# Kernel optimization log

Hardware: AMD Instinct MI355X
Metric: run time of the kernel (lower is better)

## Reference

```python
import jax, jax.numpy as jnp
import numpy as np

T, H = 4096, 2048

def _glorot(key, shape):
    return jax.random.uniform(key, shape, minval=-1.0, maxval=1.0) * jnp.sqrt(2.0 / sum(shape))

def setup_inputs() -> dict:
    key = jax.random.key(0)
    kx, ka, kb = jax.random.split(key, 3)
    x = jax.random.normal(kx, (T, H), dtype=jnp.float32)
    a_mat = _glorot(ka, (H,)).astype(jnp.float32)          # |a| < 1 -> stable recurrence
    b_mat = _glorot(kb, (H, H)).astype(jnp.float32)
    return {"x": x, "a_mat": a_mat, "b_mat": b_mat}

def reference(x, a_mat, b_mat):
    # s_t = b_mat.T @ x_t for all t, done as one GEMM: (T,H) @ (H,H)
    s = x @ b_mat  # (T, H)
    def step(h, s_t):
        h = jnp.tanh(a_mat * h + s_t)
        return h, h
    h0 = jnp.zeros_like(a_mat)
    _, h_seq = jax.lax.scan(step, h0, s)
    return h_seq  # (T, H)
```

## Files before the change

kernel.cpp:

```cpp
#include <hip/hip_runtime.h>
#include <stdint.h>
#include <stddef.h>

#define Tdim 4096
#define Hdim 2048

typedef short short8 __attribute__((ext_vector_type(8)));
typedef float floatx4 __attribute__((ext_vector_type(4)));

__device__ __forceinline__ unsigned short f2bf(float f) {
  uint32_t u = __float_as_uint(f);
  u += 0x7fffu + ((u >> 16) & 1u);
  return (unsigned short)(u >> 16);
}

__device__ __forceinline__ void load_lds16(const void* g, void* l) {
  __builtin_amdgcn_global_load_lds(
      (__attribute__((address_space(1))) unsigned int*)(uintptr_t)g,
      (__attribute__((address_space(3))) unsigned int*)l,
      16, 0, 0);
}

__device__ __forceinline__ float tanh_fast(float z) {
  float e = __expf(z + z);
  return 1.0f - __fdividef(2.0f, e + 1.0f);
}

__device__ __forceinline__ short8 lds_read8(const unsigned short* p) {
  return *(const short8*)__builtin_assume_aligned(p, 16);
}

__global__ __launch_bounds__(256) void cvt_kernel(const float* __restrict__ x,
                                                  const float* __restrict__ b,
                                                  unsigned short* __restrict__ xbf,
                                                  unsigned short* __restrict__ bt) {
  __shared__ unsigned short tile[64 * 65];
  const int t = threadIdx.x;
  if (blockIdx.x < 4096) {
    size_t i = ((size_t)blockIdx.x * 256 + t) * 8;
    float4 f0 = *(const float4*)(x + i);
    float4 f1 = *(const float4*)(x + i + 4);
    union { unsigned short u[8]; uint4 v; } o;
    o.u[0] = f2bf(f0.x); o.u[1] = f2bf(f0.y); o.u[2] = f2bf(f0.z); o.u[3] = f2bf(f0.w);
    o.u[4] = f2bf(f1.x); o.u[5] = f2bf(f1.y); o.u[6] = f2bf(f1.z); o.u[7] = f2bf(f1.w);
    *(uint4*)(xbf + i) = o.v;
    return;
  }
  const int tb = blockIdx.x - 4096;
  const int bj = tb & 31;
  const int bi = tb >> 5;
  {
    const int r0 = t >> 4, c4 = (t & 15) * 4;
#pragma unroll
    for (int p = 0; p < 4; ++p) {
      int r = r0 + p * 16;
      float4 v = *(const float4*)(b + (size_t)(bi * 64 + r) * Hdim + bj * 64 + c4);
      tile[r * 65 + c4 + 0] = f2bf(v.x);
      tile[r * 65 + c4 + 1] = f2bf(v.y);
      tile[r * 65 + c4 + 2] = f2bf(v.z);
      tile[r * 65 + c4 + 3] = f2bf(v.w);
    }
  }
  __syncthreads();
  {
    const int n = t >> 2, kq = (t & 3) * 16;
    union { unsigned short u[16]; uint4 v[2]; } o;
#pragma unroll
    for (int q = 0; q < 16; ++q) o.u[q] = tile[(kq + q) * 65 + n];
    uint4* dst = (uint4*)(bt + (size_t)(bj * 64 + n) * Hdim + bi * 64 + kq);
    dst[0] = o.v[0];
    dst[1] = o.v[1];
  }
}

__global__ __launch_bounds__(256) void gemm_scan_kernel(const unsigned short* __restrict__ A,
                                                        const unsigned short* __restrict__ Bt,
                                                        const float* __restrict__ a_mat,
                                                        float* __restrict__ out) {
  __shared__ alignas(16) union SM {
    struct {
      unsigned short sA[2][128 * 64];
      unsigned short sB[2][128 * 64];
      unsigned short sAw[2][8 * 64];
    } st;
    float s_tile[136 * 129];
  } sm;

  const int tid = threadIdx.x;
  const int bm = blockIdx.x, bn = blockIdx.y;
  const int wave = tid >> 6, lane = tid & 63;
  const int wm = (wave >> 1) * 64, wn = (wave & 1) * 64;
  const int l15 = lane & 15, quad = lane >> 4;
  const int l7 = l15 & 7;

  const int swz = ((tid & 7) ^ ((tid >> 3) & 7)) * 8;
  const unsigned short* aSrc = A + ((size_t)(bm * 128 + (tid >> 3)) * Hdim + swz);
  const unsigned short* bSrc = Bt + ((size_t)(bn * 128 + (tid >> 3)) * Hdim + swz);
  const int tw0 = (bm > 0) ? bm * 128 - 8 : 0;
  const int wswz = ((lane & 7) ^ ((lane >> 3) & 7)) * 8;
  const unsigned short* wSrc = A + ((size_t)(tw0 + (lane >> 3)) * Hdim + wswz);

  floatx4 acc[4][4] = {};
  floatx4 accw[4] = {};

  auto stage = [&](int buf, int k0) {
    unsigned short* aDst = &sm.st.sA[buf][tid * 8];
    unsigned short* bDst = &sm.st.sB[buf][tid * 8];
#pragma unroll
    for (int c = 0; c < 4; ++c)
      load_lds16(aSrc + (size_t)c * 32 * Hdim + k0, aDst + c * 2048);
#pragma unroll
    for (int c = 0; c < 4; ++c)
      load_lds16(bSrc + (size_t)c * 32 * Hdim + k0, bDst + c * 2048);
    if (wave == 3) load_lds16(wSrc + k0, &sm.st.sAw[buf][lane * 8]);
  };

  auto compute = [&](int buf) {
#pragma unroll
    for (int kk = 0; kk < 64; kk += 32) {
      const int coff = (((kk >> 3) + quad) ^ l7) * 8;
      short8 av[4], bv[4];
#pragma unroll
      for (int i = 0; i < 4; ++i)
        av[i] = lds_read8(&sm.st.sA[buf][(wm + i * 16 + l15) * 64 + coff]);
#pragma unroll
      for (int j = 0; j < 4; ++j)
        bv[j] = lds_read8(&sm.st.sB[buf][(wn + j * 16 + l15) * 64 + coff]);
#pragma unroll
      for (int i = 0; i < 4; ++i)
#pragma unroll
        for (int j = 0; j < 4; ++j)
          acc[i][j] = __builtin_amdgcn_mfma_f32_16x16x32_bf16(av[i], bv[j], acc[i][j], 0, 0, 0);
      if (wave < 2) {
        short8 aw = lds_read8(&sm.st.sAw[buf][l7 * 64 + coff]);
#pragma unroll
        for (int j = 0; j < 4; ++j)
          accw[j] = __builtin_amdgcn_mfma_f32_16x16x32_bf16(aw, bv[j], accw[j], 0, 0, 0);
      }
    }
  };

  stage(0, 0);
  __syncthreads();
  for (int it = 0; it < 32; it += 2) {
    stage(1, (it + 1) * 64);
    compute(0);
    __syncthreads();
    if (it + 2 < 32) stage(0, (it + 2) * 64);
    compute(1);
    __syncthreads();
  }

  if (wave < 2 && quad < 2) {
#pragma unroll
    for (int j = 0; j < 4; ++j)
#pragma unroll
      for (int r = 0; r < 4; ++r)
        sm.s_tile[(quad * 4 + r) * 129 + wn + j * 16 + l15] = accw[j][r];
  }
#pragma unroll
  for (int i = 0; i < 4; ++i)
#pragma unroll
    for (int j = 0; j < 4; ++j)
#pragma unroll
      for (int r = 0; r < 4; ++r)
        sm.s_tile[(8 + wm + i * 16 + quad * 4 + r) * 129 + wn + j * 16 + l15] = acc[i][j][r];
  __syncthreads();

  const int col = tid & 127;
  const int half = tid >> 7;
  const float aj = a_mat[bn * 128 + col];
  float h = 0.0f;
  const int row0 = 8 + half * 64;
  if (!(bm == 0 && half == 0)) {
#pragma unroll
    for (int r = row0 - 8; r < row0; ++r)
      h = tanh_fast(fmaf(aj, h, sm.s_tile[r * 129 + col]));
  }
  const size_t gbase = (size_t)(bm * 128 + half * 64) * Hdim + bn * 128 + col;
#pragma unroll 4
  for (int r2 = 0; r2 < 64; ++r2) {
    h = tanh_fast(fmaf(aj, h, sm.s_tile[(row0 + r2) * 129 + col]));
    out[gbase + (size_t)r2 * Hdim] = h;
  }
}

extern "C" void kernel_launch(void* const* d_in, const int* in_sizes, int n_in,
                              void* d_out, int out_size, void* d_ws, size_t ws_size,
                              hipStream_t stream) {
  const float* x = (const float*)d_in[0];
  const float* a = (const float*)d_in[1];
  const float* b = (const float*)d_in[2];
  float* out = (float*)d_out;

  unsigned short* ws = (unsigned short*)d_ws;
  unsigned short* xbf = ws;
  unsigned short* btb = xbf + (size_t)Tdim * Hdim;

  hipLaunchKernelGGL(cvt_kernel, dim3(4096 + (Hdim / 64) * (Hdim / 64)), dim3(256), 0, stream,
                     x, b, xbf, btb);
  hipLaunchKernelGGL(gemm_scan_kernel, dim3(Tdim / 128, Hdim / 128), dim3(256), 0, stream,
                     xbf, btb, a, out);
}
```

Before: 139.7 us.

## Enlarge GEMM tile to 256x128 with triple-buffered LDS pipeline and remapped grid

The fused GEMM+scan kernel moves to 512 threads with a 256x128 output tile and a three-stage LDS buffer. Global-to-LDS prefetch is split into two halves interleaved with the two k-substeps, synchronized by raw s_barrier and explicit vmcnt/lgkmcnt waits, and MFMA sections run at raised priority. Block indices are remapped to a 1D grid with a swizzle meant to improve L2 reuse. The aim is to overlap loads with MFMA work and to re-read B less often. The cost is much larger LDS use and register pressure that may limit occupancy, plus fragile hand-written wait counts.

```diff
diff --git a/kernel.cpp b/kernel.cpp
--- a/kernel.cpp
+++ b/kernel.cpp
@@ -73,83 +73,134 @@
   }
 }
 
-__global__ __launch_bounds__(256) void gemm_scan_kernel(const unsigned short* __restrict__ A,
-                                                        const unsigned short* __restrict__ Bt,
-                                                        const float* __restrict__ a_mat,
-                                                        float* __restrict__ out) {
+#define BARM() asm volatile("s_barrier" ::: "memory")
+#define WAITV(N) asm volatile("s_waitcnt vmcnt(" #N ")" ::: "memory")
+#define WAITL0() asm volatile("s_waitcnt lgkmcnt(0)" ::: "memory")
+
+__global__ __launch_bounds__(512, 2) void gemm_scan_kernel(const unsigned short* __restrict__ A,
+                                                           const unsigned short* __restrict__ Bt,
+                                                           const float* __restrict__ a_mat,
+                                                           float* __restrict__ out) {
   __shared__ alignas(16) union SM {
     struct {
-      unsigned short sA[2][128 * 64];
-      unsigned short sB[2][128 * 64];
-      unsigned short sAw[2][8 * 64];
+      unsigned short sA[3][256 * 64];
+      unsigned short sB[3][128 * 64];
+      unsigned short sAw[3][8 * 64];
     } st;
-    float s_tile[136 * 129];
+    float s_tile[264 * 129];
   } sm;
 
   const int tid = threadIdx.x;
-  const int bm = blockIdx.x, bn = blockIdx.y;
+  const int b0 = blockIdx.x;
+  const int nid = (b0 & 7) * 32 + (b0 >> 3);
+  const int bm = nid >> 4;
+  const int bn = nid & 15;
   const int wave = tid >> 6, lane = tid & 63;
   const int wm = (wave >> 1) * 64, wn = (wave & 1) * 64;
   const int l15 = lane & 15, quad = lane >> 4;
   const int l7 = l15 & 7;
 
   const int swz = ((tid & 7) ^ ((tid >> 3) & 7)) * 8;
-  const unsigned short* aSrc = A + ((size_t)(bm * 128 + (tid >> 3)) * Hdim + swz);
+  const unsigned short* aSrc = A + ((size_t)(bm * 256 + (tid >> 3)) * Hdim + swz);
   const unsigned short* bSrc = Bt + ((size_t)(bn * 128 + (tid >> 3)) * Hdim + swz);
-  const int tw0 = (bm > 0) ? bm * 128 - 8 : 0;
+  const int tw0 = (bm > 0) ? bm * 256 - 8 : 0;
   const int wswz = ((lane & 7) ^ ((lane >> 3) & 7)) * 8;
   const unsigned short* wSrc = A + ((size_t)(tw0 + (lane >> 3)) * Hdim + wswz);
 
   floatx4 acc[4][4] = {};
   floatx4 accw[4] = {};
 
-  auto stage = [&](int buf, int k0) {
-    unsigned short* aDst = &sm.st.sA[buf][tid * 8];
-    unsigned short* bDst = &sm.st.sB[buf][tid * 8];
-#pragma unroll
-    for (int c = 0; c < 4; ++c)
-      load_lds16(aSrc + (size_t)c * 32 * Hdim + k0, aDst + c * 2048);
-#pragma unroll
-    for (int c = 0; c < 4; ++c)
-      load_lds16(bSrc + (size_t)c * 32 * Hdim + k0, bDst + c * 2048);
-    if (wave == 3) load_lds16(wSrc + k0, &sm.st.sAw[buf][lane * 8]);
+  const int c0 = (quad ^ l7) * 8;
+  const int c1 = c0 ^ 32;
+  int rA[4], rB[4];
+#pragma unroll
+  for (int i = 0; i < 4; ++i) rA[i] = (wm + i * 16 + l15) * 64;
+#pragma unroll
+  for (int j = 0; j < 4; ++j) rB[j] = (wn + j * 16 + l15) * 64;
+
+  auto stage_p0 = [&](int nb, int k0) {
+    unsigned short* aDst = &sm.st.sA[nb][tid * 8];
+    load_lds16(aSrc + k0, aDst);
+    load_lds16(aSrc + (size_t)64 * Hdim + k0, aDst + 4096);
+    load_lds16(bSrc + k0, &sm.st.sB[nb][tid * 8]);
   };
-
-  auto compute = [&](int buf) {
-#pragma unroll
-    for (int kk = 0; kk < 64; kk += 32) {
-      const int coff = (((kk >> 3) + quad) ^ l7) * 8;
-      short8 av[4], bv[4];
-#pragma unroll
-      for (int i = 0; i < 4; ++i)
-        av[i] = lds_read8(&sm.st.sA[buf][(wm + i * 16 + l15) * 64 + coff]);
-#pragma unroll
-      for (int j = 0; j < 4; ++j)
-        bv[j] = lds_read8(&sm.st.sB[buf][(wn + j * 16 + l15) * 64 + coff]);
-#pragma unroll
-      for (int i = 0; i < 4; ++i)
-#pragma unroll
-        for (int j = 0; j < 4; ++j)
-          acc[i][j] = __builtin_amdgcn_mfma_f32_16x16x32_bf16(av[i], bv[j], acc[i][j], 0, 0, 0);
-      if (wave < 2) {
-        short8 aw = lds_read8(&sm.st.sAw[buf][l7 * 64 + coff]);
-#pragma unroll
-        for (int j = 0; j < 4; ++j)
-          accw[j] = __builtin_amdgcn_mfma_f32_16x16x32_bf16(aw, bv[j], accw[j], 0, 0, 0);
-      }
-    }
+  auto stage_p1 = [&](int nb, int k0) {
+    unsigned short* aDst = &sm.st.sA[nb][tid * 8];
+    load_lds16(aSrc + (size_t)128 * Hdim + k0, aDst + 8192);
+    load_lds16(aSrc + (size_t)192 * Hdim + k0, aDst + 12288);
+    load_lds16(bSrc + (size_t)64 * Hdim + k0, &sm.st.sB[nb][tid * 8 + 4096]);
+    if (wave == 7) load_lds16(wSrc + k0, &sm.st.sAw[nb][lane * 8]);
   };
 
-  stage(0, 0);
+  stage_p0(0, 0);  stage_p1(0, 0);
+  stage_p0(1, 64); stage_p1(1, 64);
+  if (wave == 7) { WAITV(7); } else { WAITV(6); }
+  BARM();
+
+  int buf = 0;
+  for (int t = 0; t < 32; ++t) {
+    const int nb = (buf >= 1) ? buf - 1 : 2;
+    const bool pf = (t < 30);
+    const int k2 = (t + 2) * 64;
+    const unsigned short* sAb = sm.st.sA[buf];
+    const unsigned short* sBb = sm.st.sB[buf];
+    const unsigned short* sWb = sm.st.sAw[buf];
+
+    short8 av[4], bv[4], aw = {};
+
+#pragma unroll
+    for (int i = 0; i < 4; ++i) av[i] = lds_read8(sAb + rA[i] + c0);
+#pragma unroll
+    for (int j = 0; j < 4; ++j) bv[j] = lds_read8(sBb + rB[j] + c0);
+    if (wave < 2) aw = lds_read8(sWb + l7 * 64 + c0);
+    if (pf) stage_p0(nb, k2);
+    BARM();
+    WAITL0();
+    __builtin_amdgcn_sched_barrier(0);
+    __builtin_amdgcn_s_setprio(1);
+#pragma unroll
+    for (int i = 0; i < 4; ++i)
+#pragma unroll
+      for (int j = 0; j < 4; ++j)
+        acc[i][j] = __builtin_amdgcn_mfma_f32_16x16x32_bf16(av[i], bv[j], acc[i][j], 0, 0, 0);
+    if (wave < 2) {
+#pragma unroll
+      for (int j = 0; j < 4; ++j)
+        accw[j] = __builtin_amdgcn_mfma_f32_16x16x32_bf16(aw, bv[j], accw[j], 0, 0, 0);
+    }
+    __builtin_amdgcn_s_setprio(0);
+    BARM();
+
+#pragma unroll
+    for (int i = 0; i < 4; ++i) av[i] = lds_read8(sAb + rA[i] + c1);
+#pragma unroll
+    for (int j = 0; j < 4; ++j) bv[j] = lds_read8(sBb + rB[j] + c1);
+    if (wave < 2) aw = lds_read8(sWb + l7 * 64 + c1);
+    if (pf) stage_p1(nb, k2);
+    BARM();
+    WAITL0();
+    __builtin_amdgcn_sched_barrier(0);
+    __builtin_amdgcn_s_setprio(1);
+#pragma unroll
+    for (int i = 0; i < 4; ++i)
+#pragma unroll
+      for (int j = 0; j < 4; ++j)
+        acc[i][j] = __builtin_amdgcn_mfma_f32_16x16x32_bf16(av[i], bv[j], acc[i][j], 0, 0, 0);
+    if (wave < 2) {
+#pragma unroll
+      for (int j = 0; j < 4; ++j)
+        accw[j] = __builtin_amdgcn_mfma_f32_16x16x32_bf16(aw, bv[j], accw[j], 0, 0, 0);
+    }
+    __builtin_amdgcn_s_setprio(0);
+    if (t < 30) {
+      if (wave == 7) { WAITV(7); } else { WAITV(6); }
+    } else if (t == 30) {
+      WAITV(0);
+    }
+    BARM();
+    buf = (buf == 2) ? 0 : buf + 1;
+  }
   __syncthreads();
-  for (int it = 0; it < 32; it += 2) {
-    stage(1, (it + 1) * 64);
-    compute(0);
-    __syncthreads();
-    if (it + 2 < 32) stage(0, (it + 2) * 64);
-    compute(1);
-    __syncthreads();
-  }
 
   if (wave < 2 && quad < 2) {
 #pragma unroll
@@ -168,16 +219,16 @@
   __syncthreads();
 
   const int col = tid & 127;
-  const int half = tid >> 7;
+  const int chunk = tid >> 7;
   const float aj = a_mat[bn * 128 + col];
   float h = 0.0f;
-  const int row0 = 8 + half * 64;
-  if (!(bm == 0 && half == 0)) {
+  const int row0 = 8 + chunk * 64;
+  if (!(bm == 0 && chunk == 0)) {
 #pragma unroll
     for (int r = row0 - 8; r < row0; ++r)
       h = tanh_fast(fmaf(aj, h, sm.s_tile[r * 129 + col]));
   }
-  const size_t gbase = (size_t)(bm * 128 + half * 64) * Hdim + bn * 128 + col;
+  const size_t gbase = (size_t)(bm * 256 + chunk * 64) * Hdim + bn * 128 + col;
 #pragma unroll 4
   for (int r2 = 0; r2 < 64; ++r2) {
     h = tanh_fast(fmaf(aj, h, sm.s_tile[(row0 + r2) * 129 + col]));
@@ -199,6 +250,6 @@
 
   hipLaunchKernelGGL(cvt_kernel, dim3(4096 + (Hdim / 64) * (Hdim / 64)), dim3(256), 0, stream,
                      x, b, xbf, btb);
-  hipLaunchKernelGGL(gemm_scan_kernel, dim3(Tdim / 128, Hdim / 128), dim3(256), 0, stream,
+  hipLaunchKernelGGL(gemm_scan_kernel, dim3((Tdim / 256) * (Hdim / 128)), dim3(512), 0, stream,
                      xbf, btb, a, out);
 }
```

New measurement: 142.2 us. Within noise of the previous version (+1.8%).

## Load B fragments directly from global into registers, drop B LDS staging

Applied to the files above, without the earlier changes.

The B operand no longer goes through LDS. Each wave reads its own B fragments straight from global memory into registers, double-buffered across k-steps, and launch bounds now request 2 blocks per CU. This halves staging LDS traffic and lets more blocks fit per CU. In exchange B is no longer shared between the two waves that use the same columns, so global and L2 traffic goes up, and the 16 extra short8 registers per thread may cause spills under the tighter occupancy bound.

```diff
diff --git a/kernel.cpp b/kernel.cpp
--- a/kernel.cpp
+++ b/kernel.cpp
@@ -27,6 +27,9 @@
 }
 
 __device__ __forceinline__ short8 lds_read8(const unsigned short* p) {
+  return *(const short8*)__builtin_assume_aligned(p, 16);
+}
+__device__ __forceinline__ short8 glb_read8(const unsigned short* p) {
   return *(const short8*)__builtin_assume_aligned(p, 16);
 }
 
@@ -73,14 +76,13 @@
   }
 }
 
-__global__ __launch_bounds__(256) void gemm_scan_kernel(const unsigned short* __restrict__ A,
-                                                        const unsigned short* __restrict__ Bt,
-                                                        const float* __restrict__ a_mat,
-                                                        float* __restrict__ out) {
+__global__ __launch_bounds__(256, 2) void gemm_scan_kernel(const unsigned short* __restrict__ A,
+                                                           const unsigned short* __restrict__ Bt,
+                                                           const float* __restrict__ a_mat,
+                                                           float* __restrict__ out) {
   __shared__ alignas(16) union SM {
     struct {
       unsigned short sA[2][128 * 64];
-      unsigned short sB[2][128 * 64];
       unsigned short sAw[2][8 * 64];
     } st;
     float s_tile[136 * 129];
@@ -95,59 +97,70 @@
 
   const int swz = ((tid & 7) ^ ((tid >> 3) & 7)) * 8;
   const unsigned short* aSrc = A + ((size_t)(bm * 128 + (tid >> 3)) * Hdim + swz);
-  const unsigned short* bSrc = Bt + ((size_t)(bn * 128 + (tid >> 3)) * Hdim + swz);
   const int tw0 = (bm > 0) ? bm * 128 - 8 : 0;
   const int wswz = ((lane & 7) ^ ((lane >> 3) & 7)) * 8;
   const unsigned short* wSrc = A + ((size_t)(tw0 + (lane >> 3)) * Hdim + wswz);
 
+  const unsigned short* bBase = Bt + ((size_t)(bn * 128 + wn + l15) * Hdim + quad * 8);
+
   floatx4 acc[4][4] = {};
   floatx4 accw[4] = {};
 
   auto stage = [&](int buf, int k0) {
     unsigned short* aDst = &sm.st.sA[buf][tid * 8];
-    unsigned short* bDst = &sm.st.sB[buf][tid * 8];
 #pragma unroll
     for (int c = 0; c < 4; ++c)
       load_lds16(aSrc + (size_t)c * 32 * Hdim + k0, aDst + c * 2048);
-#pragma unroll
-    for (int c = 0; c < 4; ++c)
-      load_lds16(bSrc + (size_t)c * 32 * Hdim + k0, bDst + c * 2048);
     if (wave == 3) load_lds16(wSrc + k0, &sm.st.sAw[buf][lane * 8]);
   };
 
-  auto compute = [&](int buf) {
+  auto loadB = [&](short8 (&dst)[8], int k0) {
+#pragma unroll
+    for (int j = 0; j < 4; ++j) {
+      const unsigned short* p = bBase + (size_t)(j * 16) * Hdim + k0;
+      dst[j * 2 + 0] = glb_read8(p);
+      dst[j * 2 + 1] = glb_read8(p + 32);
+    }
+  };
+
+  auto compute = [&](int buf, const short8 (&bv)[8]) {
 #pragma unroll
     for (int kk = 0; kk < 64; kk += 32) {
       const int coff = (((kk >> 3) + quad) ^ l7) * 8;
-      short8 av[4], bv[4];
+      const int h = kk >> 5;
+      short8 av[4];
 #pragma unroll
       for (int i = 0; i < 4; ++i)
         av[i] = lds_read8(&sm.st.sA[buf][(wm + i * 16 + l15) * 64 + coff]);
 #pragma unroll
-      for (int j = 0; j < 4; ++j)
-        bv[j] = lds_read8(&sm.st.sB[buf][(wn + j * 16 + l15) * 64 + coff]);
-#pragma unroll
       for (int i = 0; i < 4; ++i)
 #pragma unroll
         for (int j = 0; j < 4; ++j)
-          acc[i][j] = __builtin_amdgcn_mfma_f32_16x16x32_bf16(av[i], bv[j], acc[i][j], 0, 0, 0);
+          acc[i][j] = __builtin_amdgcn_mfma_f32_16x16x32_bf16(av[i], bv[j * 2 + h], acc[i][j], 0, 0, 0);
       if (wave < 2) {
         short8 aw = lds_read8(&sm.st.sAw[buf][l7 * 64 + coff]);
 #pragma unroll
         for (int j = 0; j < 4; ++j)
-          accw[j] = __builtin_amdgcn_mfma_f32_16x16x32_bf16(aw, bv[j], accw[j], 0, 0, 0);
+          accw[j] = __builtin_amdgcn_mfma_f32_16x16x32_bf16(aw, bv[j * 2 + h], accw[j], 0, 0, 0);
       }
     }
   };
 
+  short8 bv0[8], bv1[8];
+
   stage(0, 0);
+  loadB(bv0, 0);
   __syncthreads();
   for (int it = 0; it < 32; it += 2) {
     stage(1, (it + 1) * 64);
-    compute(0);
+    loadB(bv1, (it + 1) * 64);
+    compute(0, bv0);
     __syncthreads();
-    if (it + 2 < 32) stage(0, (it + 2) * 64);
-    compute(1);
+    if (it + 2 < 32) {
+      stage(0, (it + 2) * 64);
+      loadB(bv0, (it + 2) * 64);
+    }
+    compute(1, bv1);
     __syncthreads();
   }
 
```

Result: slower. 173.0 us (+23.8%).
